# Kernel optimization log

Hardware: AMD Instinct MI355X
Metric: run time of the kernel (lower is better)

Reference implementation:

```python
import jax, jax.numpy as jnp
import numpy as np

ROPE_BASE = 100.0  # croco/dust3r RoPE2D default freq


def _rope1d(tok, pos1d, base=ROPE_BASE):
    # tok: [B,H,N,D], pos1d: [B,N] int
    D = tok.shape[-1]
    half = D // 2
    inv_freq = 1.0 / (base ** (jnp.arange(0, D, 2, dtype=jnp.float32) / D))  # [D/2]
    ang = pos1d[..., None].astype(jnp.float32) * inv_freq                    # [B,N,D/2]
    ang = jnp.concatenate([ang, ang], axis=-1)                               # [B,N,D]
    cos = jnp.cos(ang)[:, None, :, :].astype(tok.dtype)  # [B,1,N,D]
    sin = jnp.sin(ang)[:, None, :, :].astype(tok.dtype)
    t1, t2 = tok[..., :half], tok[..., half:]
    rot = jnp.concatenate([-t2, t1], axis=-1)  # rotate_half
    return tok * cos + rot * sin


def rope2d(tok, pos, base=ROPE_BASE):
    # tok: [B,H,N,C], pos: [B,N,2] (y,x) integer coords
    D = tok.shape[-1] // 2
    y = _rope1d(tok[..., :D], pos[..., 0], base)
    x = _rope1d(tok[..., D:], pos[..., 1], base)
    return jnp.concatenate([y, x], axis=-1)


def setup_inputs() -> dict:
    key = jax.random.key(0)
    k1, k2, k3, k4, k5 = jax.random.split(key, 5)
    B, H, N, C = 2, 12, 2049, 64
    q = jax.random.normal(k1, (B, H, N, C), dtype=jnp.float32)
    k = jax.random.normal(k2, (B, H, N, C), dtype=jnp.float32)
    v = jax.random.normal(k3, (B, H, N, C), dtype=jnp.float32)
    qpos = jax.random.randint(k4, (B, N, 2), 0, 64, dtype=jnp.int32)
    kpos = jax.random.randint(k5, (B, N, 2), 0, 64, dtype=jnp.int32)
    mask_for_attention = jnp.ones((B, N, N), dtype=bool)
    return {"q": q, "k": k, "v": v, "qpos": qpos, "kpos": kpos,
            "mask_for_attention": mask_for_attention, "num_cls": 1}


def reference(q, k, v, qpos, kpos, mask_for_attention, num_cls):
    B, H, Nq, C = q.shape
    scale = C ** -0.5
    # split off cls tokens, apply RoPE only to positional tokens
    q_nc = rope2d(q[:, :, num_cls:], qpos[:, num_cls:])
    k_nc = rope2d(k[:, :, num_cls:], kpos[:, num_cls:])
    # block similarity matrix:
    #            | K_cls |   K_pos    |
    #   | Q_cls |        sim_qcls_k   |
    #   |       | sim_q |-------------|
    #   | Q_pos |        |  sim_rope  |
    sim_rope = jnp.einsum('bhqc,bhkc->bhqk', q_nc, k_nc)                      # [B,H,Nq-cls,Nk-cls]
    sim_qcls_k = jnp.einsum('bhqc,bhkc->bhqk', q[:, :, :num_cls], k[:, :, num_cls:])
    sim_q = jnp.einsum('bhqc,bhkc->bhqk', q, k[:, :, :num_cls])               # [B,H,Nq,cls]
    sim = jnp.concatenate([sim_qcls_k, sim_rope], axis=-2)
    sim = jnp.concatenate([sim_q, sim], axis=-1)                              # [B,H,Nq,Nk]
    sim = sim * scale
    sim = jnp.where(mask_for_attention[:, None], sim, -jnp.inf)
    attn = jax.nn.softmax(sim, axis=-1)
    x = jnp.einsum('bhqk,bhkc->bhqc', attn, v)
    return x.transpose(0, 2, 1, 3).reshape(B, Nq, C * H)
```

## Files before the change

### kernel.cpp

```cpp
#include <hip/hip_runtime.h>
#include <hip/hip_bf16.h>

typedef __attribute__((ext_vector_type(8))) short bf16x8;
typedef __attribute__((ext_vector_type(16))) float f32x16;
typedef __attribute__((ext_vector_type(4))) float f32x4;
typedef __attribute__((ext_vector_type(2))) float f32x2;
typedef unsigned short u16;

#define BN 2
#define HN 12
#define NN 2049
#define CN 64
#define NT 2048
#define BH 24
#define QSCL 0.1803368801111204f

__device__ __forceinline__ u16 f2bf(float x) {
  unsigned u = __builtin_bit_cast(unsigned, x);
  unsigned r = (u + 0x7fffu + ((u >> 16) & 1u)) >> 16;
  return (u16)r;
}

__device__ __forceinline__ unsigned cvt_pk(float lo, float hi) {
  unsigned r;
  asm("v_cvt_pk_bf16_f32 %0, %1, %2" : "=v"(r) : "v"(lo), "v"(hi));
  return r;
}

union PU {
  unsigned u[4];
  bf16x8 v;
};
union B8 {
  f32x2 h[2];
  bf16x8 v;
};

__global__ __launch_bounds__(256) void rope_pack(
    const float* __restrict__ q, const float* __restrict__ k, const float* __restrict__ v,
    const int* __restrict__ qpos, const int* __restrict__ kpos,
    u16* __restrict__ Qr, u16* __restrict__ Kr, u16* __restrict__ Vt,
    float* __restrict__ S0, float* __restrict__ Pl, float* __restrict__ Po) {
  const int bh = blockIdx.x;
  const int t = blockIdx.y;
  const int b = bh / HN;
  const int tid = threadIdx.x;
  const int wv = tid >> 6, l = tid & 63;

  __shared__ float lutc[1024], luts[1024];
  __shared__ u16 ldsV[64][36];
  __shared__ float q0s[64], k0s[64];
  __shared__ float osum[4][64];
  __shared__ float psum[4];

  const int n0 = 1 + t * 32;
  const size_t base0 = (size_t)bh * NN * CN;

  const float LF = 6.6438561897747253f / 16.0f;
  for (int i = tid; i < 1024; i += 256) {
    const int pos = i >> 4, f = i & 15;
    const float inv = exp2f(-(float)f * LF);
    float sv, cv;
    sincosf((float)pos * inv, &sv, &cv);
    lutc[i] = cv;
    luts[i] = sv;
  }
  if (tid < 64) {
    q0s[tid] = q[base0 + tid];
    k0s[tid] = k[base0 + tid];
  }
  __syncthreads();

  float oacc = 0.f, pacc = 0.f;
#pragma unroll 2
  for (int i = 0; i < 8; ++i) {
    const int tok = i * 4 + wv;
    const int c = l;
    const int n = n0 + tok;
    const size_t base = base0 + (size_t)n * CN;
    const int cp = c & 31, f = cp & 15, axis = c >> 5;
    const int qp_ = qpos[((size_t)b * NN + n) * 2 + axis];
    const int kp_ = kpos[((size_t)b * NN + n) * 2 + axis];
    const float qa = q[base + c];
    const float ka = k[base + c];
    const float qrot = (cp < 16) ? -q[base + c + 16] : q[base + c - 16];
    const float krot = (cp < 16) ? -k[base + c + 16] : k[base + c - 16];
    Qr[((size_t)bh * NT + (n - 1)) * CN + c] =
        f2bf((qa * lutc[qp_ * 16 + f] + qrot * luts[qp_ * 16 + f]) * QSCL);
    Kr[((size_t)bh * NT + (n - 1)) * CN + c] =
        f2bf(ka * lutc[kp_ * 16 + f] + krot * luts[kp_ * 16 + f]);
    const float vv = v[base + c];
    ldsV[c][tok] = f2bf(vv);

    float pk = ka * q0s[c];
    float pq = qa * k0s[c];
    pk += __shfl_xor(pk, 1, 64);  pq += __shfl_xor(pq, 1, 64);
    pk += __shfl_xor(pk, 2, 64);  pq += __shfl_xor(pq, 2, 64);
    pk += __shfl_xor(pk, 4, 64);  pq += __shfl_xor(pq, 4, 64);
    pk += __shfl_xor(pk, 8, 64);  pq += __shfl_xor(pq, 8, 64);
    pk += __shfl_xor(pk, 16, 64); pq += __shfl_xor(pq, 16, 64);
    pk += __shfl_xor(pk, 32, 64); pq += __shfl_xor(pq, 32, 64);
    const float p = __builtin_amdgcn_exp2f(pk * QSCL);
    pacc += p;
    oacc += p * vv;
    if (l == 0) S0[(size_t)bh * NT + (n - 1)] = pq * QSCL;
  }
  osum[wv][l] = oacc;
  if (l == 0) psum[wv] = pacc;
  __syncthreads();

  for (int e = tid; e < 2048; e += 256) {
    const int c = e >> 5, tok = e & 31;
    const int T = t * 32 + tok;
    const int t6 = T & 63, ch = t6 >> 3, j = t6 & 7;
    const int pos = 16 * (ch >> 1) + 4 * (ch & 1) + 8 * (j >> 2) + (j & 3);
    Vt[((size_t)bh * CN + c) * NT + (T >> 6) * 64 + pos] = ldsV[c][tok];
  }
  if (tid < 64)
    Po[(size_t)(bh * 64 + t) * 64 + tid] =
        osum[0][tid] + osum[1][tid] + osum[2][tid] + osum[3][tid];
  if (tid == 0) Pl[bh * 64 + t] = psum[0] + psum[1] + psum[2] + psum[3];
}

__global__ __launch_bounds__(64) void row0_reduce(
    const float* __restrict__ q, const float* __restrict__ k, const float* __restrict__ v,
    const float* __restrict__ Pl, const float* __restrict__ Po, float* __restrict__ out) {
  const int bh = blockIdx.x;
  const int b = bh / HN, h = bh % HN;
  const int c = threadIdx.x;
  const size_t base0 = (size_t)bh * NN * CN;
  float pr = q[base0 + c] * k[base0 + c];
  pr += __shfl_xor(pr, 1, 64);
  pr += __shfl_xor(pr, 2, 64);
  pr += __shfl_xor(pr, 4, 64);
  pr += __shfl_xor(pr, 8, 64);
  pr += __shfl_xor(pr, 16, 64);
  pr += __shfl_xor(pr, 32, 64);
  const float p00 = __builtin_amdgcn_exp2f(pr * QSCL);
  float L = p00;
  float acc = p00 * v[base0 + c];
#pragma unroll
  for (int i = 0; i < 64; ++i) {
    L += Pl[bh * 64 + i];
    acc += Po[(size_t)(bh * 64 + i) * 64 + c];
  }
  out[(size_t)b * NN * (HN * CN) + h * CN + c] = acc / L;
}

__global__ __launch_bounds__(256, 3) void attn_main(
    const float* __restrict__ v,
    const u16* __restrict__ Qr, const u16* __restrict__ Kr, const u16* __restrict__ Vt,
    const float* __restrict__ S0, float* __restrict__ out) {
  const int wg = blockIdx.x;
  const int bh = 3 * (wg & 7) + ((wg >> 3) >> 5);
  const int qt = (wg >> 3) & 31;
  const int b = bh / HN, h = bh % HN;
  const int tid = threadIdx.x;
  const int wv = tid >> 6, l = tid & 63;
  const int l31 = l & 31, lh = l >> 5;
  const int qh = wv & 1, kh = wv >> 1;

  __shared__ u16 ldsK[2][4096];
  __shared__ u16 ldsV[2][4096];
  __shared__ float v0f[64];
  __shared__ float Lbuf[64];
  float* Obuf = reinterpret_cast<float*>(&ldsK[0][0]);

  if (tid < 64) v0f[tid] = v[(size_t)bh * NN * CN + tid];
  __syncthreads();

  const int qrow = qt * 64 + qh * 32 + l31;
  const u16* qp = Qr + ((size_t)bh * NT + qrow) * CN + lh * 8;
  bf16x8 qf[4];
#pragma unroll
  for (int s = 0; s < 4; ++s) qf[s] = *reinterpret_cast<const bf16x8*>(qp + s * 16);

  const float s0l2 = S0[(size_t)bh * NT + qrow];
  const float p0 = __builtin_amdgcn_exp2f(s0l2);
  float lsum = (kh == 0 && lh == 0) ? p0 : 0.f;

  f32x16 o[2];
#pragma unroll
  for (int half = 0; half < 2; ++half)
#pragma unroll
    for (int reg = 0; reg < 16; ++reg)
      o[half][reg] =
          (kh == 0) ? p0 * v0f[(reg & 3) + 8 * (reg >> 2) + 4 * lh + 32 * half] : 0.f;

  const u16* Kbh = Kr + (size_t)bh * NT * CN;
  const u16* Vbh = Vt + (size_t)bh * CN * NT;
  char* ldsKc = reinterpret_cast<char*>(&ldsK[0][0]);
  char* ldsVc = reinterpret_cast<char*>(&ldsV[0][0]);

  const int s16 = tid & 7, srowA = tid >> 3, srowB = (tid >> 3) + 32;
  const int swA = (srowA & 15) << 3, swB = (srowB & 15) << 3;
  const int kA0 = srowA * 128 + ((s16 * 16) ^ swA);
  const int kA1 = srowA * 128 + ((s16 * 16 + 8) ^ swA);
  const int kB0 = srowB * 128 + ((s16 * 16) ^ swB);
  const int kB1 = srowB * 128 + ((s16 * 16 + 8) ^ swB);

  f32x4 kreg[2], vrg[2];
#define LOAD_TILE(nx)                                                                       \
  do {                                                                                      \
    kreg[0] = *reinterpret_cast<const f32x4*>(Kbh + (size_t)((nx) + srowA) * CN + s16 * 8); \
    kreg[1] = *reinterpret_cast<const f32x4*>(Kbh + (size_t)((nx) + srowB) * CN + s16 * 8); \
    vrg[0] = *reinterpret_cast<const f32x4*>(Vbh + (size_t)srowA * NT + (nx) + s16 * 8);    \
    vrg[1] = *reinterpret_cast<const f32x4*>(Vbh + (size_t)srowB * NT + (nx) + s16 * 8);    \
  } while (0)

#define WR2(base, off0, off1, vec4)                                           \
  do {                                                                        \
    f32x2 lo_, hi_;                                                           \
    lo_[0] = (vec4)[0]; lo_[1] = (vec4)[1];                                   \
    hi_[0] = (vec4)[2]; hi_[1] = (vec4)[3];                                   \
    *reinterpret_cast<f32x2*>((base) + (off0)) = lo_;                         \
    *reinterpret_cast<f32x2*>((base) + (off1)) = hi_;                         \
  } while (0)

#define STAGE_WRITE(bofs)                        \
  do {                                           \
    WR2(ldsKc + (bofs), kA0, kA1, kreg[0]);      \
    WR2(ldsKc + (bofs), kB0, kB1, kreg[1]);      \
    WR2(ldsVc + (bofs), kA0, kA1, vrg[0]);       \
    WR2(ldsVc + (bofs), kB0, kB1, vrg[1]);       \
  } while (0)

  LOAD_TILE(0);
  STAGE_WRITE(0);
  LOAD_TILE(64);

#pragma unroll 2
  for (int kt = 0; kt < 32; ++kt) {
    const int cur = (kt & 1) * 8192;
    const int nxt = ((kt + 1) & 1) * 8192;
    __syncthreads();
    if (kt < 31) {
      STAGE_WRITE(nxt);
      if (kt < 30) LOAD_TILE((kt + 2) * 64);
    }

    const int trow = kh * 32 + l31;
    const int tsw = (trow & 15) << 3;
    f32x16 S;
#pragma unroll
    for (int reg = 0; reg < 16; ++reg) S[reg] = 0.f;
    __builtin_amdgcn_s_setprio(1);
#pragma unroll
    for (int st = 0; st < 4; ++st) {
      B8 kb;
      const int cb = st * 32 + lh * 16;
      kb.h[0] = *reinterpret_cast<const f32x2*>(ldsKc + cur + trow * 128 + (cb ^ tsw));
      kb.h[1] = *reinterpret_cast<const f32x2*>(ldsKc + cur + trow * 128 + ((cb + 8) ^ tsw));
      S = __builtin_amdgcn_mfma_f32_32x32x16_bf16(kb.v, qf[st], S, 0, 0, 0);
    }
    __builtin_amdgcn_s_setprio(0);

    PU pa[2];
    {
      float e[16];
#pragma unroll
      for (int reg = 0; reg < 16; ++reg) e[reg] = __builtin_amdgcn_exp2f(S[reg]);
#pragma unroll
      for (int reg = 0; reg < 16; reg += 4)
        lsum += (e[reg] + e[reg + 1]) + (e[reg + 2] + e[reg + 3]);
#pragma unroll
      for (int m = 0; m < 4; ++m) {
        pa[0].u[m] = cvt_pk(e[2 * m], e[2 * m + 1]);
        pa[1].u[m] = cvt_pk(e[8 + 2 * m], e[9 + 2 * m]);
      }
    }

    __builtin_amdgcn_s_setprio(1);
#pragma unroll
    for (int half = 0; half < 2; ++half) {
      const int crow = half * 32 + l31;
      const int csw = (crow & 15) << 3;
#pragma unroll
      for (int ks = 0; ks < 2; ++ks) {
        B8 vb;
        const int pb = (kh * 2 + ks) * 32 + lh * 16;
        vb.h[0] = *reinterpret_cast<const f32x2*>(ldsVc + cur + crow * 128 + (pb ^ csw));
        vb.h[1] = *reinterpret_cast<const f32x2*>(ldsVc + cur + crow * 128 + ((pb + 8) ^ csw));
        o[half] = __builtin_amdgcn_mfma_f32_32x32x16_bf16(vb.v, pa[ks].v, o[half], 0, 0, 0);
      }
    }
    __builtin_amdgcn_s_setprio(0);
  }

  const float wls = lsum + __shfl_xor(lsum, 32, 64);
  __syncthreads();
  if (kh == 1) {
#pragma unroll
    for (int half = 0; half < 2; ++half)
#pragma unroll
      for (int reg = 0; reg < 16; ++reg) {
        const int c = (reg & 3) + 8 * (reg >> 2) + 4 * lh + 32 * half;
        Obuf[qh * 2048 + c * 32 + l31] = o[half][reg];
      }
    if (lh == 0) Lbuf[qh * 32 + l31] = wls;
  }
  __syncthreads();
  if (kh == 0) {
    const float L = wls + Lbuf[qh * 32 + l31];
    const float invl = 1.0f / L;
    const int n = 1 + qrow;
    float* op = out + ((size_t)b * NN + n) * (HN * CN) + h * CN;
#pragma unroll
    for (int half = 0; half < 2; ++half) {
#pragma unroll
      for (int rg = 0; rg < 4; ++rg) {
        f32x4 val;
#pragma unroll
        for (int j = 0; j < 4; ++j) {
          const int reg = 4 * rg + j;
          const int c = (reg & 3) + 8 * (reg >> 2) + 4 * lh + 32 * half;
          val[j] = (o[half][reg] + Obuf[qh * 2048 + c * 32 + l31]) * invl;
        }
        *reinterpret_cast<f32x4*>(op + 8 * rg + 4 * lh + 32 * half) = val;
      }
    }
  }
#undef LOAD_TILE
#undef WR2
#undef STAGE_WRITE
}

extern "C" void kernel_launch(void* const* d_in, const int* in_sizes, int n_in,
                              void* d_out, int out_size, void* d_ws, size_t ws_size,
                              hipStream_t stream) {
  const float* q = (const float*)d_in[0];
  const float* k = (const float*)d_in[1];
  const float* v = (const float*)d_in[2];
  const int* qpos = (const int*)d_in[3];
  const int* kpos = (const int*)d_in[4];
  float* out = (float*)d_out;

  u16* Qr = (u16*)d_ws;
  u16* Kr = Qr + (size_t)BH * NT * CN;
  u16* Vt = Kr + (size_t)BH * NT * CN;
  float* S0 = (float*)(Vt + (size_t)BH * NT * CN);
  float* Pl = S0 + (size_t)BH * NT;
  float* Po = Pl + BH * 64;

  rope_pack<<<dim3(BH, 64), 256, 0, stream>>>(q, k, v, qpos, kpos, Qr, Kr, Vt, S0, Pl, Po);
  attn_main<<<dim3(BH * 32), 256, 0, stream>>>(v, Qr, Kr, Vt, S0, out);
  row0_reduce<<<dim3(BH), 64, 0, stream>>>(q, k, v, Pl, Po, out);
}
```

Measured before the change: 61.41 us.

## Split attention KV range across two workgroups and merge partials in new kernel

Each query tile's key range is split in two halves handled by separate workgroups (split-K / flash-decoding style), doubling the grid from 768 to 1536 workgroups so the device's compute units are better filled. Unnormalized partial outputs and row sums go to workspace and a new merge kernel sums them and normalizes. Occupancy hint raised from 3 to 4 waves per SIMD. Costs an extra kernel launch plus writing and rereading partial outputs through global memory; safe without max-rescaling since softmax uses no running max.

```diff
diff --git a/kernel.cpp b/kernel.cpp
--- a/kernel.cpp
+++ b/kernel.cpp
@@ -147,14 +147,17 @@
   out[(size_t)b * NN * (HN * CN) + h * CN + c] = acc / L;
 }
 
-__global__ __launch_bounds__(256, 3) void attn_main(
+__global__ __launch_bounds__(256, 4) void attn_main(
     const float* __restrict__ v,
     const u16* __restrict__ Qr, const u16* __restrict__ Kr, const u16* __restrict__ Vt,
-    const float* __restrict__ S0, float* __restrict__ out) {
+    const float* __restrict__ S0, float* __restrict__ Op, float* __restrict__ Lp) {
   const int wg = blockIdx.x;
-  const int bh = 3 * (wg & 7) + ((wg >> 3) >> 5);
-  const int qt = (wg >> 3) & 31;
-  const int b = bh / HN, h = bh % HN;
+  const int inner = wg >> 3;
+  const int bh = 3 * (wg & 7) + inner / 64;
+  const int rem = inner & 63;
+  const int qt = rem >> 1;
+  const int zt = rem & 1;
+  const int kt0 = zt << 4;
   const int tid = threadIdx.x;
   const int wv = tid >> 6, l = tid & 63;
   const int l31 = l & 31, lh = l >> 5;
@@ -176,16 +179,17 @@
   for (int s = 0; s < 4; ++s) qf[s] = *reinterpret_cast<const bf16x8*>(qp + s * 16);
 
   const float s0l2 = S0[(size_t)bh * NT + qrow];
-  const float p0 = __builtin_amdgcn_exp2f(s0l2);
-  float lsum = (kh == 0 && lh == 0) ? p0 : 0.f;
+  const float p0 = (zt == 0) ? __builtin_amdgcn_exp2f(s0l2) : 0.f;
+  float lsum = (zt == 0 && kh == 0 && lh == 0) ? p0 : 0.f;
 
   f32x16 o[2];
 #pragma unroll
   for (int half = 0; half < 2; ++half)
 #pragma unroll
     for (int reg = 0; reg < 16; ++reg)
-      o[half][reg] =
-          (kh == 0) ? p0 * v0f[(reg & 3) + 8 * (reg >> 2) + 4 * lh + 32 * half] : 0.f;
+      o[half][reg] = (zt == 0 && kh == 0)
+                         ? p0 * v0f[(reg & 3) + 8 * (reg >> 2) + 4 * lh + 32 * half]
+                         : 0.f;
 
   const u16* Kbh = Kr + (size_t)bh * NT * CN;
   const u16* Vbh = Vt + (size_t)bh * CN * NT;
@@ -225,18 +229,19 @@
     WR2(ldsVc + (bofs), kB0, kB1, vrg[1]);       \
   } while (0)
 
-  LOAD_TILE(0);
+  LOAD_TILE(kt0 * 64);
   STAGE_WRITE(0);
-  LOAD_TILE(64);
+  LOAD_TILE((kt0 + 1) * 64);
 
 #pragma unroll 2
-  for (int kt = 0; kt < 32; ++kt) {
-    const int cur = (kt & 1) * 8192;
-    const int nxt = ((kt + 1) & 1) * 8192;
+  for (int t = 0; t < 16; ++t) {
+    const int kt = kt0 + t;
+    const int cur = (t & 1) * 8192;
+    const int nxt = ((t + 1) & 1) * 8192;
     __syncthreads();
-    if (kt < 31) {
+    if (t < 15) {
       STAGE_WRITE(nxt);
-      if (kt < 30) LOAD_TILE((kt + 2) * 64);
+      if (t < 14) LOAD_TILE((kt + 2) * 64);
     }
 
     const int trow = kh * 32 + l31;
@@ -302,9 +307,9 @@
   __syncthreads();
   if (kh == 0) {
     const float L = wls + Lbuf[qh * 32 + l31];
-    const float invl = 1.0f / L;
-    const int n = 1 + qrow;
-    float* op = out + ((size_t)b * NN + n) * (HN * CN) + h * CN;
+    const int pi = (bh * 32 + qt) * 2 + zt;
+    const int ql = qh * 32 + l31;
+    float* opart = Op + (size_t)pi * 4096 + ql * 64;
 #pragma unroll
     for (int half = 0; half < 2; ++half) {
 #pragma unroll
@@ -314,15 +319,40 @@
         for (int j = 0; j < 4; ++j) {
           const int reg = 4 * rg + j;
           const int c = (reg & 3) + 8 * (reg >> 2) + 4 * lh + 32 * half;
-          val[j] = (o[half][reg] + Obuf[qh * 2048 + c * 32 + l31]) * invl;
+          val[j] = o[half][reg] + Obuf[qh * 2048 + c * 32 + l31];
         }
-        *reinterpret_cast<f32x4*>(op + 8 * rg + 4 * lh + 32 * half) = val;
+        *reinterpret_cast<f32x4*>(opart + 8 * rg + 4 * lh + 32 * half) = val;
       }
     }
+    if (lh == 0) Lp[pi * 64 + ql] = L;
   }
 #undef LOAD_TILE
 #undef WR2
 #undef STAGE_WRITE
+}
+
+__global__ __launch_bounds__(256) void attn_merge(
+    const float* __restrict__ Op, const float* __restrict__ Lp, float* __restrict__ out) {
+  const int bh = blockIdx.x, qt = blockIdx.y;
+  const int b = bh / HN, h = bh % HN;
+  const int tid = threadIdx.x;
+  const int ql = tid >> 2;
+  const int cg = (tid & 3) * 16;
+  const int pi = (bh * 32 + qt) * 2;
+  const float L = Lp[pi * 64 + ql] + Lp[(pi + 1) * 64 + ql];
+  const float invl = 1.0f / L;
+  const float* o0 = Op + (size_t)pi * 4096 + ql * 64 + cg;
+  const float* o1 = o0 + 4096;
+  float* op = out + ((size_t)b * NN + 1 + qt * 64 + ql) * (HN * CN) + h * CN + cg;
+#pragma unroll
+  for (int j = 0; j < 16; j += 4) {
+    f32x4 a = *reinterpret_cast<const f32x4*>(o0 + j);
+    f32x4 bb = *reinterpret_cast<const f32x4*>(o1 + j);
+    f32x4 r;
+#pragma unroll
+    for (int jj = 0; jj < 4; ++jj) r[jj] = (a[jj] + bb[jj]) * invl;
+    *reinterpret_cast<f32x4*>(op + j) = r;
+  }
 }
 
 extern "C" void kernel_launch(void* const* d_in, const int* in_sizes, int n_in,
@@ -341,8 +371,11 @@
   float* S0 = (float*)(Vt + (size_t)BH * NT * CN);
   float* Pl = S0 + (size_t)BH * NT;
   float* Po = Pl + BH * 64;
+  float* Op = Po + (size_t)BH * 64 * 64;
+  float* Lp = Op + (size_t)1536 * 4096;
 
   rope_pack<<<dim3(BH, 64), 256, 0, stream>>>(q, k, v, qpos, kpos, Qr, Kr, Vt, S0, Pl, Po);
-  attn_main<<<dim3(BH * 32), 256, 0, stream>>>(v, Qr, Kr, Vt, S0, out);
+  attn_main<<<dim3(1536), 256, 0, stream>>>(v, Qr, Kr, Vt, S0, Op, Lp);
+  attn_merge<<<dim3(BH, 32), 256, 0, stream>>>(Op, Lp, out);
   row0_reduce<<<dim3(BH), 64, 0, stream>>>(q, k, v, Pl, Po, out);
 }
```

Result: slower. 92.33 us (+50.4%).

## Stream K/V tiles into LDS with global_load_lds and pre-swizzled global layout

Applied to the files above, without the earlier changes.

The attention kernel's K and V tile staging, which went global memory to registers to LDS, is replaced by direct global-to-LDS loads via global_load_lds. Because that path cannot apply a per-lane LDS swizzle, the preprocessing kernel now writes Kr and Vt to global memory with the XOR swizzle already applied. The goal is to cut register pressure and the VGPR round trip and LDS write instructions in the main loop. The trade-off is a shorter prefetch distance, one tile ahead instead of two, and a reliance on the compiler waiting correctly for the asynchronous LDS loads before the barrier.

```diff
diff --git a/kernel.cpp b/kernel.cpp
--- a/kernel.cpp
+++ b/kernel.cpp
@@ -87,7 +87,8 @@
     const float krot = (cp < 16) ? -k[base + c + 16] : k[base + c - 16];
     Qr[((size_t)bh * NT + (n - 1)) * CN + c] =
         f2bf((qa * lutc[qp_ * 16 + f] + qrot * luts[qp_ * 16 + f]) * QSCL);
-    Kr[((size_t)bh * NT + (n - 1)) * CN + c] =
+    const int rsw = ((n - 1) & 15) << 2;
+    Kr[((size_t)bh * NT + (n - 1)) * CN + (c ^ rsw)] =
         f2bf(ka * lutc[kp_ * 16 + f] + krot * luts[kp_ * 16 + f]);
     const float vv = v[base + c];
     ldsV[c][tok] = f2bf(vv);
@@ -114,7 +115,7 @@
     const int T = t * 32 + tok;
     const int t6 = T & 63, ch = t6 >> 3, j = t6 & 7;
     const int pos = 16 * (ch >> 1) + 4 * (ch & 1) + 8 * (j >> 2) + (j & 3);
-    Vt[((size_t)bh * CN + c) * NT + (T >> 6) * 64 + pos] = ldsV[c][tok];
+    Vt[((size_t)bh * CN + c) * NT + (T >> 6) * 64 + (pos ^ ((c & 15) << 2))] = ldsV[c][tok];
   }
   if (tid < 64)
     Po[(size_t)(bh * 64 + t) * 64 + tid] =
@@ -193,51 +194,39 @@
   char* ldsVc = reinterpret_cast<char*>(&ldsV[0][0]);
 
   const int s16 = tid & 7, srowA = tid >> 3, srowB = (tid >> 3) + 32;
-  const int swA = (srowA & 15) << 3, swB = (srowB & 15) << 3;
-  const int kA0 = srowA * 128 + ((s16 * 16) ^ swA);
-  const int kA1 = srowA * 128 + ((s16 * 16 + 8) ^ swA);
-  const int kB0 = srowB * 128 + ((s16 * 16) ^ swB);
-  const int kB1 = srowB * 128 + ((s16 * 16 + 8) ^ swB);
-
-  f32x4 kreg[2], vrg[2];
-#define LOAD_TILE(nx)                                                                       \
-  do {                                                                                      \
-    kreg[0] = *reinterpret_cast<const f32x4*>(Kbh + (size_t)((nx) + srowA) * CN + s16 * 8); \
-    kreg[1] = *reinterpret_cast<const f32x4*>(Kbh + (size_t)((nx) + srowB) * CN + s16 * 8); \
-    vrg[0] = *reinterpret_cast<const f32x4*>(Vbh + (size_t)srowA * NT + (nx) + s16 * 8);    \
-    vrg[1] = *reinterpret_cast<const f32x4*>(Vbh + (size_t)srowB * NT + (nx) + s16 * 8);    \
+
+#define DMA_TILE(nx, bofs)                                                                   \
+  do {                                                                                       \
+    __builtin_amdgcn_global_load_lds(                                                        \
+        (const __attribute__((address_space(1))) unsigned int*)(Kbh +                        \
+            (size_t)((nx) + srowA) * CN + s16 * 8),                                          \
+        (__attribute__((address_space(3))) unsigned int*)(ldsKc + (bofs) + wv * 1024),       \
+        16, 0, 0);                                                                           \
+    __builtin_amdgcn_global_load_lds(                                                        \
+        (const __attribute__((address_space(1))) unsigned int*)(Kbh +                        \
+            (size_t)((nx) + srowB) * CN + s16 * 8),                                          \
+        (__attribute__((address_space(3))) unsigned int*)(ldsKc + (bofs) + 4096 + wv * 1024),\
+        16, 0, 0);                                                                           \
+    __builtin_amdgcn_global_load_lds(                                                        \
+        (const __attribute__((address_space(1))) unsigned int*)(Vbh +                        \
+            (size_t)srowA * NT + (nx) + s16 * 8),                                            \
+        (__attribute__((address_space(3))) unsigned int*)(ldsVc + (bofs) + wv * 1024),       \
+        16, 0, 0);                                                                           \
+    __builtin_amdgcn_global_load_lds(                                                        \
+        (const __attribute__((address_space(1))) unsigned int*)(Vbh +                        \
+            (size_t)srowB * NT + (nx) + s16 * 8),                                            \
+        (__attribute__((address_space(3))) unsigned int*)(ldsVc + (bofs) + 4096 + wv * 1024),\
+        16, 0, 0);                                                                           \
   } while (0)
 
-#define WR2(base, off0, off1, vec4)                                           \
-  do {                                                                        \
-    f32x2 lo_, hi_;                                                           \
-    lo_[0] = (vec4)[0]; lo_[1] = (vec4)[1];                                   \
-    hi_[0] = (vec4)[2]; hi_[1] = (vec4)[3];                                   \
-    *reinterpret_cast<f32x2*>((base) + (off0)) = lo_;                         \
-    *reinterpret_cast<f32x2*>((base) + (off1)) = hi_;                         \
-  } while (0)
-
-#define STAGE_WRITE(bofs)                        \
-  do {                                           \
-    WR2(ldsKc + (bofs), kA0, kA1, kreg[0]);      \
-    WR2(ldsKc + (bofs), kB0, kB1, kreg[1]);      \
-    WR2(ldsVc + (bofs), kA0, kA1, vrg[0]);       \
-    WR2(ldsVc + (bofs), kB0, kB1, vrg[1]);       \
-  } while (0)
-
-  LOAD_TILE(0);
-  STAGE_WRITE(0);
-  LOAD_TILE(64);
+  DMA_TILE(0, 0);
 
 #pragma unroll 2
   for (int kt = 0; kt < 32; ++kt) {
     const int cur = (kt & 1) * 8192;
     const int nxt = ((kt + 1) & 1) * 8192;
     __syncthreads();
-    if (kt < 31) {
-      STAGE_WRITE(nxt);
-      if (kt < 30) LOAD_TILE((kt + 2) * 64);
-    }
+    if (kt < 31) DMA_TILE((kt + 1) * 64, nxt);
 
     const int trow = kh * 32 + l31;
     const int tsw = (trow & 15) << 3;
@@ -320,9 +309,7 @@
       }
     }
   }
-#undef LOAD_TILE
-#undef WR2
-#undef STAGE_WRITE
+#undef DMA_TILE
 }
 
 extern "C" void kernel_launch(void* const* d_in, const int* in_sizes, int n_in,
```

Result: no change. 61.09 us, median of 2 (-0.5%).
